# Kernel tuning notes

Hardware: AMD Instinct MI355X
Metric: run time of the kernel (lower is better)

## Reference

```python
import jax, jax.numpy as jnp
import numpy as np

BLOCK_SIZE = 256

def setup_inputs() -> dict:
    key = jax.random.key(0)
    ks = jax.random.split(key, 5)
    B, T, C, H = 256, 256, 512, 64
    return {
        "x": jax.random.normal(ks[0], (B, T, C), dtype=jnp.float32),
        "y": jax.random.normal(ks[1], (B, T, C), dtype=jnp.float32),
        "Wq": jax.random.normal(ks[2], (C, H), dtype=jnp.float32) * (C ** -0.5),
        "Wk": jax.random.normal(ks[3], (C, H), dtype=jnp.float32) * (C ** -0.5),
        "Wv": jax.random.normal(ks[4], (C, H), dtype=jnp.float32) * (C ** -0.5),
    }

def reference(x, y, Wq, Wk, Wv):
    # q/k/v projections (Linear without bias): [B,T,C] @ [C,H] -> [B,T,H]
    q = jnp.einsum('btc,ch->bth', x, Wq)
    k = jnp.einsum('btc,ch->bth', y, Wk)
    v = jnp.einsum('btc,ch->bth', y, Wv)
    head_size = k.shape[-1]
    # scaled dot-product scores: [B,T,T]
    wei = jnp.einsum('bth,bsh->bts', q, k) * (head_size ** -0.5)
    # causal mask (is_causal=True): lower-triangular allowed
    T = x.shape[1]
    causal = jnp.tril(jnp.ones((T, T), dtype=bool))
    wei = jnp.where(causal, wei, -jnp.inf)
    wei = jax.nn.softmax(wei, axis=-1)
    # dropout omitted (eval mode / identity)
    out = jnp.einsum('bts,bsh->bth', wei, v)
    return out
```

## Files before the change

### kernel.cpp

```cpp
#include <hip/hip_runtime.h>


typedef _Float16 half8 __attribute__((ext_vector_type(8)));
typedef float floatx4 __attribute__((ext_vector_type(4)));

#define MFMA16(a, b, c) __builtin_amdgcn_mfma_f32_16x16x32_f16((a), (b), (c), 0, 0, 0)

__device__ inline half8 cvt8(float4 a, float4 b) {
  half8 r;
  r[0] = (_Float16)a.x; r[1] = (_Float16)a.y; r[2] = (_Float16)a.z; r[3] = (_Float16)a.w;
  r[4] = (_Float16)b.x; r[5] = (_Float16)b.y; r[6] = (_Float16)b.z; r[7] = (_Float16)b.w;
  return r;
}

template <int NOUT>
__global__ __launch_bounds__(256) void proj_kernel(
    const float* __restrict__ X, const float* __restrict__ W0,
    const float* __restrict__ W1, _Float16* __restrict__ O0,
    _Float16* __restrict__ O1) {
  __shared__ _Float16 a_lds[128][40];
  __shared__ _Float16 w_lds[NOUT][64][40];

  const int tid = threadIdx.x;
  const int row0 = blockIdx.x * 128;
  const int wv = tid >> 6;
  const int lane = tid & 63;
  const int l15 = lane & 15, quad = lane >> 4;

  floatx4 acc[2][4 * NOUT];
#pragma unroll
  for (int i = 0; i < 2; i++)
#pragma unroll
    for (int j = 0; j < 4 * NOUT; j++) acc[i][j] = (floatx4)0.f;

  const int arow = tid >> 1;
  const int ahalf = (tid & 1) * 16;
  const int wkk = tid >> 3;
  const int wn0 = (tid & 7) * 8;

  for (int k0 = 0; k0 < 512; k0 += 32) {
    {
      const float4* s4 = (const float4*)(X + (size_t)(row0 + arow) * 512 + k0 + ahalf);
      float4 f0 = s4[0], f1 = s4[1], f2 = s4[2], f3 = s4[3];
      *(half8*)&a_lds[arow][ahalf]     = cvt8(f0, f1);
      *(half8*)&a_lds[arow][ahalf + 8] = cvt8(f2, f3);
    }
#pragma unroll
    for (int wi = 0; wi < NOUT; wi++) {
      const float* wsrc = (wi ? W1 : W0) + (size_t)(k0 + wkk) * 64 + wn0;
      float4 g0 = ((const float4*)wsrc)[0];
      float4 g1 = ((const float4*)wsrc)[1];
      w_lds[wi][wn0 + 0][wkk] = (_Float16)g0.x;
      w_lds[wi][wn0 + 1][wkk] = (_Float16)g0.y;
      w_lds[wi][wn0 + 2][wkk] = (_Float16)g0.z;
      w_lds[wi][wn0 + 3][wkk] = (_Float16)g0.w;
      w_lds[wi][wn0 + 4][wkk] = (_Float16)g1.x;
      w_lds[wi][wn0 + 5][wkk] = (_Float16)g1.y;
      w_lds[wi][wn0 + 6][wkk] = (_Float16)g1.z;
      w_lds[wi][wn0 + 7][wkk] = (_Float16)g1.w;
    }
    __syncthreads();
    half8 af0 = *(const half8*)&a_lds[wv * 32 + l15][quad * 8];
    half8 af1 = *(const half8*)&a_lds[wv * 32 + 16 + l15][quad * 8];
#pragma unroll
    for (int wi = 0; wi < NOUT; wi++)
#pragma unroll
      for (int j = 0; j < 4; j++) {
        half8 bf = *(const half8*)&w_lds[wi][j * 16 + l15][quad * 8];
        acc[0][wi * 4 + j] = MFMA16(af0, bf, acc[0][wi * 4 + j]);
        acc[1][wi * 4 + j] = MFMA16(af1, bf, acc[1][wi * 4 + j]);
      }
    __syncthreads();
  }
#pragma unroll
  for (int i = 0; i < 2; i++)
#pragma unroll
    for (int wi = 0; wi < NOUT; wi++) {
      _Float16* O = wi ? O1 : O0;
#pragma unroll
      for (int j = 0; j < 4; j++)
#pragma unroll
        for (int r = 0; r < 4; r++) {
          int grow = row0 + wv * 32 + i * 16 + quad * 4 + r;
          O[(size_t)grow * 64 + j * 16 + l15] = (_Float16)acc[i][wi * 4 + j][r];
        }
    }
}

__global__ __launch_bounds__(256) void attn_kernel(
    const _Float16* __restrict__ Qw, const _Float16* __restrict__ Kw,
    const _Float16* __restrict__ Vw, float* __restrict__ Out) {
  __shared__ _Float16 k_lds[64][72];
  __shared__ _Float16 vt_lds[64][72];
  __shared__ _Float16 p_lds[4][16][72];

  const int qt = blockIdx.x, bb = blockIdx.y;
  const int tid = threadIdx.x;
  const int wv = tid >> 6;
  const int lane = tid & 63;
  const int l15 = lane & 15, quad = lane >> 4;
  const float SCALE = 0.125f * 1.4426950408889634f;
  const float NEG = -3.0e38f;

  const size_t qoff = ((size_t)bb * 256 + qt * 64 + wv * 16 + l15) * 64 + quad * 8;
  half8 qf0 = *(const half8*)(Qw + qoff);
  half8 qf1 = *(const half8*)(Qw + qoff + 32);

  floatx4 o[4];
#pragma unroll
  for (int t = 0; t < 4; t++) o[t] = (floatx4)0.f;
  float mrow[4], lrow[4];
#pragma unroll
  for (int r = 0; r < 4; r++) { mrow[r] = NEG; lrow[r] = 0.f; }

  const int srow = tid >> 2;
  const int sc = (tid & 3) * 16;

  for (int j = 0; j <= qt; j++) {
    __syncthreads();
    {
      const size_t base = ((size_t)bb * 256 + j * 64 + srow) * 64 + sc;
      const half8* ksrc = (const half8*)(Kw + base);
      half8 ka = ksrc[0], kb = ksrc[1];
      *(half8*)&k_lds[srow][sc]     = ka;
      *(half8*)&k_lds[srow][sc + 8] = kb;
      const half8* vsrc = (const half8*)(Vw + base);
      half8 va = vsrc[0], vb = vsrc[1];
#pragma unroll
      for (int e = 0; e < 8; e++) vt_lds[sc + e][srow] = va[e];
#pragma unroll
      for (int e = 0; e < 8; e++) vt_lds[sc + 8 + e][srow] = vb[e];
    }
    __syncthreads();

    floatx4 sacc[4];
#pragma unroll
    for (int t = 0; t < 4; t++) sacc[t] = (floatx4)0.f;
#pragma unroll
    for (int t = 0; t < 4; t++) {
      half8 b0 = *(const half8*)&k_lds[t * 16 + l15][quad * 8];
      sacc[t] = MFMA16(qf0, b0, sacc[t]);
      half8 b1 = *(const half8*)&k_lds[t * 16 + l15][32 + quad * 8];
      sacc[t] = MFMA16(qf1, b1, sacc[t]);
    }

    float y[4][4];
#pragma unroll
    for (int t = 0; t < 4; t++)
#pragma unroll
      for (int r = 0; r < 4; r++) y[t][r] = sacc[t][r] * SCALE;
    if (j == qt) {
#pragma unroll
      for (int t = 0; t < 4; t++)
#pragma unroll
        for (int r = 0; r < 4; r++)
          if (t * 16 + l15 > wv * 16 + quad * 4 + r) y[t][r] = NEG;
    }

#pragma unroll
    for (int r = 0; r < 4; r++) {
      float mx = fmaxf(fmaxf(y[0][r], y[1][r]), fmaxf(y[2][r], y[3][r]));
#pragma unroll
      for (int off = 1; off < 16; off <<= 1) mx = fmaxf(mx, __shfl_xor(mx, off, 64));
      float mnew = fmaxf(mrow[r], mx);
      float al = exp2f(mrow[r] - mnew);
      mrow[r] = mnew;
      float rs = 0.f;
#pragma unroll
      for (int t = 0; t < 4; t++) {
        float p = exp2f(y[t][r] - mnew);
        y[t][r] = p;
        rs += p;
      }
#pragma unroll
      for (int off = 1; off < 16; off <<= 1) rs += __shfl_xor(rs, off, 64);
      lrow[r] = lrow[r] * al + rs;
      o[0][r] *= al; o[1][r] *= al; o[2][r] *= al; o[3][r] *= al;
    }

#pragma unroll
    for (int t = 0; t < 4; t++)
#pragma unroll
      for (int r = 0; r < 4; r++)
        p_lds[wv][quad * 4 + r][t * 16 + l15] = (_Float16)y[t][r];
    __syncthreads();

#pragma unroll
    for (int ss = 0; ss < 2; ss++) {
      half8 pa = *(const half8*)&p_lds[wv][l15][ss * 32 + quad * 8];
#pragma unroll
      for (int th = 0; th < 4; th++) {
        half8 vb = *(const half8*)&vt_lds[th * 16 + l15][ss * 32 + quad * 8];
        o[th] = MFMA16(pa, vb, o[th]);
      }
    }
  }

#pragma unroll
  for (int th = 0; th < 4; th++)
#pragma unroll
    for (int r = 0; r < 4; r++) {
      int grow = qt * 64 + wv * 16 + quad * 4 + r;
      Out[((size_t)bb * 256 + grow) * 64 + th * 16 + l15] = o[th][r] / lrow[r];
    }
}

extern "C" void kernel_launch(void* const* d_in, const int* in_sizes, int n_in,
                              void* d_out, int out_size, void* d_ws, size_t ws_size,
                              hipStream_t stream) {
  const float* x  = (const float*)d_in[0];
  const float* y  = (const float*)d_in[1];
  const float* Wq = (const float*)d_in[2];
  const float* Wk = (const float*)d_in[3];
  const float* Wv = (const float*)d_in[4];
  float* out = (float*)d_out;

  _Float16* qw = (_Float16*)d_ws;
  _Float16* kw = qw + (size_t)65536 * 64;
  _Float16* vw = kw + (size_t)65536 * 64;

  proj_kernel<1><<<512, 256, 0, stream>>>(x, Wq, nullptr, qw, nullptr);
  proj_kernel<2><<<512, 256, 0, stream>>>(y, Wk, Wv, kw, vw);
  attn_kernel<<<dim3(4, 256), 256, 0, stream>>>(qw, kw, vw, out);
}
```

Baseline: 318.2 us.

## Pre-transpose weights to fp16, drop LDS staging, emit V transposed

Adds a small kernel that converts and transposes the three weight matrices to fp16 once per call. The projection kernel then reads X straight into MFMA fragments and fetches weight fragments from global memory, with no LDS staging and no barriers in the K loop. The K/V projection writes V already transposed per batch, so the attention kernel can load K and V fragments directly from global memory and drop its LDS tiles and two of its barriers. This trades LDS traffic and synchronisation for uncoalesced, L2-dependent global fragment loads and one extra kernel launch.

New measurement: 349.3 us. +9.8%, slower.

```diff
diff --git a/kernel.cpp b/kernel.cpp
--- a/kernel.cpp
+++ b/kernel.cpp
@@ -13,13 +13,41 @@
   return r;
 }
 
+__global__ __launch_bounds__(256) void wt_kernel(
+    const float* __restrict__ Wq, const float* __restrict__ Wk,
+    const float* __restrict__ Wv, _Float16* __restrict__ Wt) {
+  __shared__ _Float16 t_lds[64][72];
+  const int w = blockIdx.x >> 3, kb = blockIdx.x & 7;
+  const float* W = (w == 0) ? Wq : (w == 1 ? Wk : Wv);
+  const int tid = threadIdx.x;
+  const int kk = tid >> 2;
+  const int n0 = (tid & 3) * 16;
+  const float4* src = (const float4*)(W + (size_t)(kb * 64 + kk) * 64 + n0);
+  float4 f0 = src[0], f1 = src[1], f2 = src[2], f3 = src[3];
+  t_lds[n0 +  0][kk] = (_Float16)f0.x; t_lds[n0 +  1][kk] = (_Float16)f0.y;
+  t_lds[n0 +  2][kk] = (_Float16)f0.z; t_lds[n0 +  3][kk] = (_Float16)f0.w;
+  t_lds[n0 +  4][kk] = (_Float16)f1.x; t_lds[n0 +  5][kk] = (_Float16)f1.y;
+  t_lds[n0 +  6][kk] = (_Float16)f1.z; t_lds[n0 +  7][kk] = (_Float16)f1.w;
+  t_lds[n0 +  8][kk] = (_Float16)f2.x; t_lds[n0 +  9][kk] = (_Float16)f2.y;
+  t_lds[n0 + 10][kk] = (_Float16)f2.z; t_lds[n0 + 11][kk] = (_Float16)f2.w;
+  t_lds[n0 + 12][kk] = (_Float16)f3.x; t_lds[n0 + 13][kk] = (_Float16)f3.y;
+  t_lds[n0 + 14][kk] = (_Float16)f3.z; t_lds[n0 + 15][kk] = (_Float16)f3.w;
+  __syncthreads();
+  const int n = tid >> 2;
+  const int koff = (tid & 3) * 16;
+  half8 h0 = *(const half8*)&t_lds[n][koff];
+  half8 h1 = *(const half8*)&t_lds[n][koff + 8];
+  _Float16* dst = Wt + (size_t)(w * 64 + n) * 512 + kb * 64 + koff;
+  *(half8*)dst = h0;
+  *(half8*)(dst + 8) = h1;
+}
+
 template <int NOUT>
-__global__ __launch_bounds__(256) void proj_kernel(
-    const float* __restrict__ X, const float* __restrict__ W0,
-    const float* __restrict__ W1, _Float16* __restrict__ O0,
-    _Float16* __restrict__ O1) {
-  __shared__ _Float16 a_lds[128][40];
-  __shared__ _Float16 w_lds[NOUT][64][40];
+__global__ __launch_bounds__(256, 2) void proj_kernel(
+    const float* __restrict__ X, const _Float16* __restrict__ Wt0,
+    const _Float16* __restrict__ Wt1, _Float16* __restrict__ O0,
+    _Float16* __restrict__ O1t) {
+  __shared__ _Float16 vt_tile[NOUT == 2 ? 64 : 1][NOUT == 2 ? 136 : 1];
 
   const int tid = threadIdx.x;
   const int row0 = blockIdx.x * 128;
@@ -33,65 +61,62 @@
 #pragma unroll
     for (int j = 0; j < 4 * NOUT; j++) acc[i][j] = (floatx4)0.f;
 
-  const int arow = tid >> 1;
-  const int ahalf = (tid & 1) * 16;
-  const int wkk = tid >> 3;
-  const int wn0 = (tid & 7) * 8;
-
+  const float* xr0 = X + (size_t)(row0 + wv * 32 + l15) * 512 + quad * 8;
+  const float* xr1 = xr0 + 16 * 512;
+
+#pragma unroll
   for (int k0 = 0; k0 < 512; k0 += 32) {
-    {
-      const float4* s4 = (const float4*)(X + (size_t)(row0 + arow) * 512 + k0 + ahalf);
-      float4 f0 = s4[0], f1 = s4[1], f2 = s4[2], f3 = s4[3];
-      *(half8*)&a_lds[arow][ahalf]     = cvt8(f0, f1);
-      *(half8*)&a_lds[arow][ahalf + 8] = cvt8(f2, f3);
-    }
+    float4 a0 = *(const float4*)(xr0 + k0);
+    float4 a1 = *(const float4*)(xr0 + k0 + 4);
+    float4 a2 = *(const float4*)(xr1 + k0);
+    float4 a3 = *(const float4*)(xr1 + k0 + 4);
+    half8 af0 = cvt8(a0, a1);
+    half8 af1 = cvt8(a2, a3);
 #pragma unroll
     for (int wi = 0; wi < NOUT; wi++) {
-      const float* wsrc = (wi ? W1 : W0) + (size_t)(k0 + wkk) * 64 + wn0;
-      float4 g0 = ((const float4*)wsrc)[0];
-      float4 g1 = ((const float4*)wsrc)[1];
-      w_lds[wi][wn0 + 0][wkk] = (_Float16)g0.x;
-      w_lds[wi][wn0 + 1][wkk] = (_Float16)g0.y;
-      w_lds[wi][wn0 + 2][wkk] = (_Float16)g0.z;
-      w_lds[wi][wn0 + 3][wkk] = (_Float16)g0.w;
-      w_lds[wi][wn0 + 4][wkk] = (_Float16)g1.x;
-      w_lds[wi][wn0 + 5][wkk] = (_Float16)g1.y;
-      w_lds[wi][wn0 + 6][wkk] = (_Float16)g1.z;
-      w_lds[wi][wn0 + 7][wkk] = (_Float16)g1.w;
-    }
-    __syncthreads();
-    half8 af0 = *(const half8*)&a_lds[wv * 32 + l15][quad * 8];
-    half8 af1 = *(const half8*)&a_lds[wv * 32 + 16 + l15][quad * 8];
-#pragma unroll
-    for (int wi = 0; wi < NOUT; wi++)
+      const _Float16* wp = (wi ? Wt1 : Wt0) + k0 + quad * 8;
 #pragma unroll
       for (int j = 0; j < 4; j++) {
-        half8 bf = *(const half8*)&w_lds[wi][j * 16 + l15][quad * 8];
+        half8 bf = *(const half8*)(wp + (size_t)(j * 16 + l15) * 512);
         acc[0][wi * 4 + j] = MFMA16(af0, bf, acc[0][wi * 4 + j]);
         acc[1][wi * 4 + j] = MFMA16(af1, bf, acc[1][wi * 4 + j]);
       }
+    }
+  }
+
+#pragma unroll
+  for (int i = 0; i < 2; i++)
+#pragma unroll
+    for (int j = 0; j < 4; j++)
+#pragma unroll
+      for (int r = 0; r < 4; r++) {
+        int grow = row0 + wv * 32 + i * 16 + quad * 4 + r;
+        O0[(size_t)grow * 64 + j * 16 + l15] = (_Float16)acc[i][j][r];
+      }
+  if constexpr (NOUT == 2) {
+#pragma unroll
+    for (int i = 0; i < 2; i++)
+#pragma unroll
+      for (int j = 0; j < 4; j++)
+#pragma unroll
+        for (int r = 0; r < 4; r++) {
+          int tl = wv * 32 + i * 16 + quad * 4 + r;
+          vt_tile[j * 16 + l15][tl] = (_Float16)acc[i][4 + j][r];
+        }
     __syncthreads();
+    const int b = row0 >> 8, t0 = row0 & 255;
+    const int h = tid >> 2;
+    const int seg = (tid & 3) * 32;
+    _Float16* dst = O1t + ((size_t)b * 64 + h) * 256 + t0 + seg;
+#pragma unroll
+    for (int e = 0; e < 4; e++)
+      *(half8*)(dst + e * 8) = *(const half8*)&vt_tile[h][seg + e * 8];
   }
-#pragma unroll
-  for (int i = 0; i < 2; i++)
-#pragma unroll
-    for (int wi = 0; wi < NOUT; wi++) {
-      _Float16* O = wi ? O1 : O0;
-#pragma unroll
-      for (int j = 0; j < 4; j++)
-#pragma unroll
-        for (int r = 0; r < 4; r++) {
-          int grow = row0 + wv * 32 + i * 16 + quad * 4 + r;
-          O[(size_t)grow * 64 + j * 16 + l15] = (_Float16)acc[i][wi * 4 + j][r];
-        }
-    }
 }
 
 __global__ __launch_bounds__(256) void attn_kernel(
     const _Float16* __restrict__ Qw, const _Float16* __restrict__ Kw,
-    const _Float16* __restrict__ Vw, float* __restrict__ Out) {
-  __shared__ _Float16 k_lds[64][72];
-  __shared__ _Float16 vt_lds[64][72];
+    const _Float16* __restrict__ Vt, float* __restrict__ Out) {
   __shared__ _Float16 p_lds[4][16][72];
 
   const int qt = blockIdx.x, bb = blockIdx.y;
@@ -113,36 +138,29 @@
 #pragma unroll
   for (int r = 0; r < 4; r++) { mrow[r] = NEG; lrow[r] = 0.f; }
 
-  const int srow = tid >> 2;
-  const int sc = (tid & 3) * 16;
+  const _Float16* Kb = Kw + (size_t)bb * 256 * 64;
+  const _Float16* Vb = Vt + (size_t)bb * 64 * 256;
 
   for (int j = 0; j <= qt; j++) {
-    __syncthreads();
-    {
-      const size_t base = ((size_t)bb * 256 + j * 64 + srow) * 64 + sc;
-      const half8* ksrc = (const half8*)(Kw + base);
-      half8 ka = ksrc[0], kb = ksrc[1];
-      *(half8*)&k_lds[srow][sc]     = ka;
-      *(half8*)&k_lds[srow][sc + 8] = kb;
-      const half8* vsrc = (const half8*)(Vw + base);
-      half8 va = vsrc[0], vb = vsrc[1];
-#pragma unroll
-      for (int e = 0; e < 8; e++) vt_lds[sc + e][srow] = va[e];
-#pragma unroll
-      for (int e = 0; e < 8; e++) vt_lds[sc + 8 + e][srow] = vb[e];
-    }
-    __syncthreads();
-
     floatx4 sacc[4];
 #pragma unroll
     for (int t = 0; t < 4; t++) sacc[t] = (floatx4)0.f;
 #pragma unroll
     for (int t = 0; t < 4; t++) {
-      half8 b0 = *(const half8*)&k_lds[t * 16 + l15][quad * 8];
+      const _Float16* kp = Kb + (size_t)(j * 64 + t * 16 + l15) * 64 + quad * 8;
+      half8 b0 = *(const half8*)kp;
+      half8 b1 = *(const half8*)(kp + 32);
       sacc[t] = MFMA16(qf0, b0, sacc[t]);
-      half8 b1 = *(const half8*)&k_lds[t * 16 + l15][32 + quad * 8];
       sacc[t] = MFMA16(qf1, b1, sacc[t]);
     }
+
+    half8 vb[2][4];
+#pragma unroll
+    for (int ss = 0; ss < 2; ss++)
+#pragma unroll
+      for (int th = 0; th < 4; th++)
+        vb[ss][th] = *(const half8*)(Vb + (size_t)(th * 16 + l15) * 256 +
+                                     j * 64 + ss * 32 + quad * 8);
 
     float y[4][4];
 #pragma unroll
@@ -183,16 +201,12 @@
 #pragma unroll
       for (int r = 0; r < 4; r++)
         p_lds[wv][quad * 4 + r][t * 16 + l15] = (_Float16)y[t][r];
-    __syncthreads();
 
 #pragma unroll
     for (int ss = 0; ss < 2; ss++) {
       half8 pa = *(const half8*)&p_lds[wv][l15][ss * 32 + quad * 8];
 #pragma unroll
-      for (int th = 0; th < 4; th++) {
-        half8 vb = *(const half8*)&vt_lds[th * 16 + l15][ss * 32 + quad * 8];
-        o[th] = MFMA16(pa, vb, o[th]);
-      }
+      for (int th = 0; th < 4; th++) o[th] = MFMA16(pa, vb[ss][th], o[th]);
     }
   }
 
@@ -217,9 +231,12 @@
 
   _Float16* qw = (_Float16*)d_ws;
   _Float16* kw = qw + (size_t)65536 * 64;
-  _Float16* vw = kw + (size_t)65536 * 64;
-
-  proj_kernel<1><<<512, 256, 0, stream>>>(x, Wq, nullptr, qw, nullptr);
-  proj_kernel<2><<<512, 256, 0, stream>>>(y, Wk, Wv, kw, vw);
-  attn_kernel<<<dim3(4, 256), 256, 0, stream>>>(qw, kw, vw, out);
-}
+  _Float16* vt = kw + (size_t)65536 * 64;
+  _Float16* wt = vt + (size_t)65536 * 64;
+
+  wt_kernel<<<24, 256, 0, stream>>>(Wq, Wk, Wv, wt);
+  proj_kernel<1><<<512, 256, 0, stream>>>(x, wt, nullptr, qw, nullptr);
+  proj_kernel<2><<<512, 256, 0, stream>>>(y, wt + (size_t)64 * 512,
+                                          wt + (size_t)2 * 64 * 512, kw, vt);
+  attn_kernel<<<dim3(4, 256), 256, 0, stream>>>(qw, kw, vt, out);
+}
```

## Write V transposed in projection and load K/V fragments directly from global

Applied to the files above, without the earlier changes.

The K/V projection kernel now stages the V result through shared memory and writes it in a transposed [B,H,T] layout. The attention kernel drops its shared-memory staging of K and V, along with the block-wide barriers around it, and loads MFMA operand fragments straight from global memory (relying on L1/L2). This removes the strided LDS transpose and two syncthreads per tile. The cost is redundant global loads across the four waves and an extra LDS pass plus barrier in the projection epilogue. The barrier before the P read is also removed, which is safe only because each wave reads back only its own p_lds slice.

Measured after the change: 328.8 us. +3.4%, slower.

```diff
diff --git a/kernel.cpp b/kernel.cpp
--- a/kernel.cpp
+++ b/kernel.cpp
@@ -17,9 +17,10 @@
 __global__ __launch_bounds__(256) void proj_kernel(
     const float* __restrict__ X, const float* __restrict__ W0,
     const float* __restrict__ W1, _Float16* __restrict__ O0,
-    _Float16* __restrict__ O1) {
+    _Float16* __restrict__ O1t) {
   __shared__ _Float16 a_lds[128][40];
   __shared__ _Float16 w_lds[NOUT][64][40];
+  __shared__ _Float16 vt_tile[NOUT == 2 ? 64 : 1][NOUT == 2 ? 136 : 1];
 
   const int tid = threadIdx.x;
   const int row0 = blockIdx.x * 128;
@@ -75,23 +76,36 @@
 #pragma unroll
   for (int i = 0; i < 2; i++)
 #pragma unroll
-    for (int wi = 0; wi < NOUT; wi++) {
-      _Float16* O = wi ? O1 : O0;
+    for (int j = 0; j < 4; j++)
+#pragma unroll
+      for (int r = 0; r < 4; r++) {
+        int grow = row0 + wv * 32 + i * 16 + quad * 4 + r;
+        O0[(size_t)grow * 64 + j * 16 + l15] = (_Float16)acc[i][j][r];
+      }
+  if constexpr (NOUT == 2) {
+#pragma unroll
+    for (int i = 0; i < 2; i++)
 #pragma unroll
       for (int j = 0; j < 4; j++)
 #pragma unroll
         for (int r = 0; r < 4; r++) {
-          int grow = row0 + wv * 32 + i * 16 + quad * 4 + r;
-          O[(size_t)grow * 64 + j * 16 + l15] = (_Float16)acc[i][wi * 4 + j][r];
+          int tl = wv * 32 + i * 16 + quad * 4 + r;
+          vt_tile[j * 16 + l15][tl] = (_Float16)acc[i][4 + j][r];
         }
-    }
+    __syncthreads();
+    const int b = row0 >> 8, t0 = row0 & 255;
+    const int h = tid >> 2;
+    const int seg = (tid & 3) * 32;
+    _Float16* dst = O1t + ((size_t)b * 64 + h) * 256 + t0 + seg;
+#pragma unroll
+    for (int e = 0; e < 4; e++)
+      *(half8*)(dst + e * 8) = *(const half8*)&vt_tile[h][seg + e * 8];
+  }
 }
 
 __global__ __launch_bounds__(256) void attn_kernel(
     const _Float16* __restrict__ Qw, const _Float16* __restrict__ Kw,
-    const _Float16* __restrict__ Vw, float* __restrict__ Out) {
-  __shared__ _Float16 k_lds[64][72];
-  __shared__ _Float16 vt_lds[64][72];
+    const _Float16* __restrict__ Vt, float* __restrict__ Out) {
   __shared__ _Float16 p_lds[4][16][72];
 
   const int qt = blockIdx.x, bb = blockIdx.y;
@@ -113,36 +127,29 @@
 #pragma unroll
   for (int r = 0; r < 4; r++) { mrow[r] = NEG; lrow[r] = 0.f; }
 
-  const int srow = tid >> 2;
-  const int sc = (tid & 3) * 16;
+  const _Float16* Kb = Kw + (size_t)bb * 256 * 64;
+  const _Float16* Vb = Vt + (size_t)bb * 64 * 256;
 
   for (int j = 0; j <= qt; j++) {
-    __syncthreads();
-    {
-      const size_t base = ((size_t)bb * 256 + j * 64 + srow) * 64 + sc;
-      const half8* ksrc = (const half8*)(Kw + base);
-      half8 ka = ksrc[0], kb = ksrc[1];
-      *(half8*)&k_lds[srow][sc]     = ka;
-      *(half8*)&k_lds[srow][sc + 8] = kb;
-      const half8* vsrc = (const half8*)(Vw + base);
-      half8 va = vsrc[0], vb = vsrc[1];
-#pragma unroll
-      for (int e = 0; e < 8; e++) vt_lds[sc + e][srow] = va[e];
-#pragma unroll
-      for (int e = 0; e < 8; e++) vt_lds[sc + 8 + e][srow] = vb[e];
-    }
-    __syncthreads();
-
     floatx4 sacc[4];
 #pragma unroll
     for (int t = 0; t < 4; t++) sacc[t] = (floatx4)0.f;
 #pragma unroll
     for (int t = 0; t < 4; t++) {
-      half8 b0 = *(const half8*)&k_lds[t * 16 + l15][quad * 8];
+      const _Float16* kp = Kb + (size_t)(j * 64 + t * 16 + l15) * 64 + quad * 8;
+      half8 b0 = *(const half8*)kp;
+      half8 b1 = *(const half8*)(kp + 32);
       sacc[t] = MFMA16(qf0, b0, sacc[t]);
-      half8 b1 = *(const half8*)&k_lds[t * 16 + l15][32 + quad * 8];
       sacc[t] = MFMA16(qf1, b1, sacc[t]);
     }
+
+    half8 vb[2][4];
+#pragma unroll
+    for (int ss = 0; ss < 2; ss++)
+#pragma unroll
+      for (int th = 0; th < 4; th++)
+        vb[ss][th] = *(const half8*)(Vb + (size_t)(th * 16 + l15) * 256 +
+                                     j * 64 + ss * 32 + quad * 8);
 
     float y[4][4];
 #pragma unroll
@@ -183,16 +190,12 @@
 #pragma unroll
       for (int r = 0; r < 4; r++)
         p_lds[wv][quad * 4 + r][t * 16 + l15] = (_Float16)y[t][r];
-    __syncthreads();
 
 #pragma unroll
     for (int ss = 0; ss < 2; ss++) {
       half8 pa = *(const half8*)&p_lds[wv][l15][ss * 32 + quad * 8];
 #pragma unroll
-      for (int th = 0; th < 4; th++) {
-        half8 vb = *(const half8*)&vt_lds[th * 16 + l15][ss * 32 + quad * 8];
-        o[th] = MFMA16(pa, vb, o[th]);
-      }
+      for (int th = 0; th < 4; th++) o[th] = MFMA16(pa, vb[ss][th], o[th]);
     }
   }
 
@@ -217,9 +220,9 @@
 
   _Float16* qw = (_Float16*)d_ws;
   _Float16* kw = qw + (size_t)65536 * 64;
-  _Float16* vw = kw + (size_t)65536 * 64;
+  _Float16* vt = kw + (size_t)65536 * 64;
 
   proj_kernel<1><<<512, 256, 0, stream>>>(x, Wq, nullptr, qw, nullptr);
-  proj_kernel<2><<<512, 256, 0, stream>>>(y, Wk, Wv, kw, vw);
-  attn_kernel<<<dim3(4, 256), 256, 0, stream>>>(qw, kw, vw, out);
-}
+  proj_kernel<2><<<512, 256, 0, stream>>>(y, Wk, Wv, kw, vt);
+  attn_kernel<<<dim3(4, 256), 256, 0, stream>>>(qw, kw, vt, out);
+}
```
